# Kernel tuning notes

Measured on AMD Instinct MI355X. Metric: run time of the kernel, lower is better.

The kernel has to match this reference:

```python
import jax, jax.numpy as jnp
import numpy as np

EMBED_DIM = 1024
NUM_HEADS = 16
HEAD_DIM = EMBED_DIM // NUM_HEADS
BATCH = 4
SEQ = 2048


def setup_inputs() -> dict:
    key = jax.random.key(0)
    ks = jax.random.split(key, 9)
    s = 1.0 / np.sqrt(EMBED_DIM)
    return {
        "query": jax.random.normal(ks[0], (BATCH, SEQ, EMBED_DIM), jnp.float32),
        "Wq": jax.random.normal(ks[1], (EMBED_DIM, EMBED_DIM), jnp.float32) * s,
        "bq": jnp.zeros((EMBED_DIM,), jnp.float32),
        "Wk": jax.random.normal(ks[2], (EMBED_DIM, EMBED_DIM), jnp.float32) * s,
        "bk": jnp.zeros((EMBED_DIM,), jnp.float32),
        "Wv": jax.random.normal(ks[3], (EMBED_DIM, EMBED_DIM), jnp.float32) * s,
        "bv": jnp.zeros((EMBED_DIM,), jnp.float32),
        "Wo": jax.random.normal(ks[4], (EMBED_DIM, EMBED_DIM), jnp.float32) * s,
        "bo": jnp.zeros((EMBED_DIM,), jnp.float32),
    }


def reference(query, Wq, bq, Wk, bk, Wv, bv, Wo, bo):
    bsz, seq, embed_dim = query.shape
    scaling = HEAD_DIM ** (-0.5)
    # projections (torch Linear: x @ W.T + b)
    q = (query @ Wq.T + bq) * scaling
    k = query @ Wk.T + bk
    v = query @ Wv.T + bv
    # [b, h, s, d]
    q = q.reshape(bsz, seq, NUM_HEADS, HEAD_DIM).transpose(0, 2, 1, 3)
    k = k.reshape(bsz, seq, NUM_HEADS, HEAD_DIM).transpose(0, 2, 1, 3)
    v = v.reshape(bsz, seq, NUM_HEADS, HEAD_DIM).transpose(0, 2, 1, 3)
    # full [b, h, s, s] scores (faithful to the naive original)
    scores = jnp.einsum("bhqd,bhkd->bhqk", q, k)
    causal = jnp.tril(jnp.ones((seq, seq), bool))  # [s, s]
    scores = jnp.where(causal[None, None], scores, -jnp.inf)
    probs = jax.nn.softmax(scores, axis=-1)
    attn = jnp.einsum("bhqk,bhkd->bhqd", probs, v)
    attn = attn.transpose(0, 2, 1, 3).reshape(bsz, seq, embed_dim)
    return attn @ Wo.T + bo
```

## Files before the change

kernel.cpp:

```cpp
#include <hip/hip_runtime.h>
#include <stdint.h>

typedef unsigned short u16;
typedef __attribute__((ext_vector_type(8))) __bf16 bf16x8;
typedef __attribute__((ext_vector_type(4))) float f32x4;

#define SEQL 2048
#define NHEADS 16
#define HDIM 64
#define BSZ 4
#define EMB 1024
#define MROWS (BSZ * SEQL)
#define LOG2E 1.44269504088896f
#define NKT 32

__device__ __forceinline__ u16 f2bf(float f) {
  union { float f; uint32_t u; } v; v.f = f;
  return (u16)((v.u + 0x7fffu + ((v.u >> 16) & 1u)) >> 16);
}

__device__ __forceinline__ void g2l(const u16* g, u16* l) {
  __builtin_amdgcn_global_load_lds(
      (__attribute__((address_space(1))) void*)(g),
      (__attribute__((address_space(3))) void*)(l), 16, 0, 0);
}

__device__ __forceinline__ void cvt8(const float* __restrict__ in, u16* __restrict__ out, int i) {
  float4 a = *(const float4*)(in + i);
  float4 b = *(const float4*)(in + i + 4);
  uint4 o;
  o.x = f2bf(a.x) | ((uint32_t)f2bf(a.y) << 16);
  o.y = f2bf(a.z) | ((uint32_t)f2bf(a.w) << 16);
  o.z = f2bf(b.x) | ((uint32_t)f2bf(b.y) << 16);
  o.w = f2bf(b.z) | ((uint32_t)f2bf(b.w) << 16);
  *(uint4*)(out + i) = o;
}

#define XN (MROWS * EMB)
__global__ void cvt_all(const float* __restrict__ query,
                        const float* __restrict__ w0, const float* __restrict__ w1,
                        const float* __restrict__ w2, const float* __restrict__ w3,
                        u16* __restrict__ Xb, u16* __restrict__ Wqb) {
  int i = (blockIdx.x * blockDim.x + threadIdx.x) * 8;
  if (i < XN) {
    cvt8(query, Xb, i);
  } else {
    int j = i - XN;
    int w = j >> 20;
    int jj = j & 1048575;
    const float* src = w == 0 ? w0 : w == 1 ? w1 : w == 2 ? w2 : w3;
    cvt8(src, Wqb + ((size_t)w << 20), jj);
  }
}

#define GBODY3(WSTR, RBUF, DOPF, PFT, WBUF)                                         \
  {                                                                                 \
    asm volatile("s_waitcnt " WSTR ::: "memory");                                   \
    __builtin_amdgcn_sched_barrier(0);                                              \
    __builtin_amdgcn_s_barrier();                                                   \
    __builtin_amdgcn_sched_barrier(0);                                              \
    if (DOPF) {                                                                     \
      u16* d = lds + (WBUF) * 12288;                                                \
      g2l(Agb + (PFT) * 32, d + tid * 8);                                           \
      g2l(Bgb0 + (PFT) * 32, d + 4096 + tid * 8);                                   \
      g2l(Bgb1 + (PFT) * 32, d + 8192 + tid * 8);                                   \
    }                                                                               \
    const u16* Ab = lds + (RBUF) * 12288;                                           \
    const u16* Bb = Ab + 4096;                                                      \
    bf16x8 af[4], bfr[4];                                                           \
    _Pragma("unroll") for (int i = 0; i < 4; ++i) {                                 \
      af[i] = *(const bf16x8*)(Ab + (wr * 64 + i * 16 + lrow) * 32 + kg);           \
      bfr[i] = *(const bf16x8*)(Bb + (wc * 64 + i * 16 + lrow) * 32 + kg);          \
    }                                                                               \
    __builtin_amdgcn_s_setprio(1);                                                  \
    _Pragma("unroll") for (int mi = 0; mi < 4; ++mi)                                \
      _Pragma("unroll") for (int ni = 0; ni < 4; ++ni)                              \
        acc[mi][ni] =                                                               \
            __builtin_amdgcn_mfma_f32_16x16x32_bf16(af[mi], bfr[ni], acc[mi][ni],   \
                                                    0, 0, 0);                       \
    __builtin_amdgcn_s_setprio(0);                                                  \
  }

__device__ __forceinline__ void gemm_core256(const u16* __restrict__ A,
                                             const u16* __restrict__ B,
                                             int m0, int n0, u16* lds,
                                             f32x4 acc[4][4]) {
  const int tid = threadIdx.x;
  const int lane = tid & 63, wid = tid >> 6;
  const int wr = wid >> 2, wc = wid & 3;
  const int lrow = lane & 15, kg = (lane >> 4) * 8;
  const int srow = tid >> 2, scolE = (tid & 3) * 8;

  const u16* Agb  = A + (size_t)(m0 + srow) * EMB + scolE;
  const u16* Bgb0 = B + (size_t)(n0 + srow) * EMB + scolE;
  const u16* Bgb1 = B + (size_t)(n0 + 128 + srow) * EMB + scolE;

#pragma unroll
  for (int t = 0; t < 2; ++t) {
    u16* d = lds + t * 12288;
    g2l(Agb + t * 32, d + tid * 8);
    g2l(Bgb0 + t * 32, d + 4096 + tid * 8);
    g2l(Bgb1 + t * 32, d + 8192 + tid * 8);
  }

  int rb = 0;
#pragma unroll 1
  for (int kt = 0; kt < NKT - 2; ++kt) {
    int wb = rb + 2; if (wb >= 3) wb -= 3;
    GBODY3("vmcnt(3)", rb, true, kt + 2, wb)
    ++rb; if (rb == 3) rb = 0;
  }
  GBODY3("vmcnt(3)", rb, false, 0, 0)
  { int rb2 = rb + 1; if (rb2 == 3) rb2 = 0;
    GBODY3("vmcnt(0)", rb2, false, 0, 0) }
}

__global__ __launch_bounds__(512, 4) void gemm_qkv3(
    const u16* __restrict__ X, const u16* __restrict__ Wcat,
    const float* __restrict__ bq, const float* __restrict__ bk, const float* __restrict__ bv,
    u16* __restrict__ Qb, u16* __restrict__ Kb, u16* __restrict__ Vt) {
  __shared__ u16 lds[3 * 12288];
  const int orig = blockIdx.x;
  const int virt = (orig & 7) * 96 + (orig >> 3);
  const int mt = virt / 12, nt = virt % 12;

  const f32x4 fzero = {0.f, 0.f, 0.f, 0.f};
  f32x4 acc[4][4];
#pragma unroll
  for (int i = 0; i < 4; ++i)
#pragma unroll
    for (int j = 0; j < 4; ++j) acc[i][j] = fzero;

  gemm_core256(X, Wcat, mt * 128, nt * 256, lds, acc);

  const int tid = threadIdx.x, lane = tid & 63, wid = tid >> 6;
  const int wr = wid >> 2, wc = wid & 3;
  const int lrow = lane & 15, g = lane >> 4;
  const int which = nt >> 2;
  const float* bias = which == 0 ? bq : which == 1 ? bk : bv;
  const float scale = which == 0 ? 0.125f * LOG2E : 1.0f;

  if (which == 2) {
#pragma unroll
    for (int mi = 0; mi < 4; ++mi)
#pragma unroll
      for (int ni = 0; ni < 4; ++ni) {
        int n = nt * 256 + wc * 64 + ni * 16 + lrow;
        int nn = n & 1023;
        float bs = bias[nn];
        int h = nn >> 6, d = nn & 63;
        int m0r = mt * 128 + wr * 64 + mi * 16 + g * 4;
        int b = m0r >> 11, s = m0r & 2047;
        union { u16 s4[4]; uint2 u; } o;
#pragma unroll
        for (int r = 0; r < 4; ++r) o.s4[r] = f2bf(acc[mi][ni][r] + bs);
        *(uint2*)(Vt + ((size_t)(b * NHEADS + h) * HDIM + d) * SEQL + s) = o.u;
      }
  } else {
    u16* Ob = which == 0 ? Qb : Kb;
#pragma unroll
    for (int mi = 0; mi < 4; ++mi)
#pragma unroll
      for (int ni = 0; ni < 4; ++ni) {
        int n = nt * 256 + wc * 64 + ni * 16 + lrow;
        int nn = n & 1023;
        float bs = bias[nn];
        int h = nn >> 6, d = nn & 63;
#pragma unroll
        for (int r = 0; r < 4; ++r) {
          int m = mt * 128 + wr * 64 + mi * 16 + g * 4 + r;
          int b = m >> 11, s = m & 2047;
          float v = (acc[mi][ni][r] + bs) * scale;
          Ob[(size_t)((b * NHEADS + h) * SEQL + s) * HDIM + d] = f2bf(v);
        }
      }
  }
}

__global__ __launch_bounds__(512, 4) void gemm_out2(
    const u16* __restrict__ Ain, const u16* __restrict__ Wo,
    const float* __restrict__ bo, float* __restrict__ out) {
  __shared__ u16 lds[3 * 12288];
  const int orig = blockIdx.x;
  const int virt = (orig & 7) * 32 + (orig >> 3);
  const int mt = virt >> 2, nt = virt & 3;

  const f32x4 fzero = {0.f, 0.f, 0.f, 0.f};
  f32x4 acc[4][4];
#pragma unroll
  for (int i = 0; i < 4; ++i)
#pragma unroll
    for (int j = 0; j < 4; ++j) acc[i][j] = fzero;

  gemm_core256(Ain, Wo, mt * 128, nt * 256, lds, acc);

  const int tid = threadIdx.x, lane = tid & 63, wid = tid >> 6;
  const int wr = wid >> 2, wc = wid & 3;
  const int lrow = lane & 15, g = lane >> 4;
#pragma unroll
  for (int mi = 0; mi < 4; ++mi)
#pragma unroll
    for (int ni = 0; ni < 4; ++ni) {
      int n = nt * 256 + wc * 64 + ni * 16 + lrow;
      float bs = bo[n];
#pragma unroll
      for (int r = 0; r < 4; ++r) {
        int m = mt * 128 + wr * 64 + mi * 16 + g * 4 + r;
        out[(size_t)m * EMB + n] = acc[mi][ni][r] + bs;
      }
    }
}

__device__ __forceinline__ int swz(int row, int colE) {
  return row * 64 + (colE ^ ((row & 7) << 3));
}

__global__ __launch_bounds__(512, 4) void attn6_kernel(
    const u16* __restrict__ Qb, const u16* __restrict__ Kb, const u16* __restrict__ Vt,
    u16* __restrict__ Ab) {
  __shared__ u16 Ks[2][64 * 64];
  __shared__ u16 Vs[2][64 * 64];

  const int bid = blockIdx.x;
  const int qa  = bid >> 6;
  const int bh  = bid & 63;

  const int tid = threadIdx.x, lane = tid & 63, wid = tid >> 6;
  const int lrow = lane & 15, g = lane >> 4, kg = g * 8;

  const u16* Qbh = Qb + (size_t)bh * SEQL * HDIM;
  const u16* Kbh = Kb + (size_t)bh * SEQL * HDIM;
  const u16* Vbh = Vt + (size_t)bh * HDIM * SEQL;

  const int srow = tid >> 3;
  const int sce  = (tid & 7) * 8;

  const f32x4 fzero = {0.f, 0.f, 0.f, 0.f};
  const int b = bh >> 4, h = bh & 15;

#pragma unroll 1
  for (int ph = 0; ph < 2; ++ph) {
    const int qt = ph ? (15 - qa) : qa;
    const int q0 = qt * 128;
    const int NT = 2 * (qt + 1);

    const int qrow = q0 + wid * 16 + lrow;
    const bf16x8 qf0 = *(const bf16x8*)(Qbh + (size_t)qrow * HDIM + kg);
    const bf16x8 qf1 = *(const bf16x8*)(Qbh + (size_t)qrow * HDIM + 32 + kg);

    float m_run = -1e30f, l_run = 0.f;
    f32x4 accO[4];
#pragma unroll
    for (int d = 0; d < 4; ++d) accO[d] = fzero;

    {
      uint4 k0 = *(const uint4*)(Kbh + (size_t)srow * HDIM + sce);
      uint4 v0 = *(const uint4*)(Vbh + (size_t)srow * SEQL + sce);
      *(uint4*)(&Ks[0][swz(srow, sce)]) = k0;
      *(uint4*)(&Vs[0][swz(srow, sce)]) = v0;
    }
    __syncthreads();

    for (int t = 0; t < NT; ++t) {
      const int cur = t & 1;
      const int kv0 = t * 64;
      const bool pf = (t + 1 < NT);
      uint4 k0, v0;
      if (pf) {
        const int kvn = kv0 + 64;
        k0 = *(const uint4*)(Kbh + (size_t)(kvn + srow) * HDIM + sce);
        v0 = *(const uint4*)(Vbh + (size_t)srow * SEQL + kvn + sce);
      }

      f32x4 sacc[4];
      __builtin_amdgcn_s_setprio(1);
#pragma unroll
      for (int kb = 0; kb < 4; ++kb) {
        bf16x8 kfa = *(const bf16x8*)(&Ks[cur][swz(kb * 16 + lrow, kg)]);
        bf16x8 kfb = *(const bf16x8*)(&Ks[cur][swz(kb * 16 + lrow, 32 + kg)]);
        f32x4 z = fzero;
        z = __builtin_amdgcn_mfma_f32_16x16x32_bf16(kfa, qf0, z, 0, 0, 0);
        z = __builtin_amdgcn_mfma_f32_16x16x32_bf16(kfb, qf1, z, 0, 0, 0);
        sacc[kb] = z;
      }
      __builtin_amdgcn_s_setprio(0);

      if (kv0 + 63 > q0 + wid * 16) {
#pragma unroll
        for (int kb = 0; kb < 4; ++kb)
#pragma unroll
          for (int r = 0; r < 4; ++r)
            if (kv0 + kb * 16 + g * 4 + r > qrow) sacc[kb][r] = -1e30f;
      }

      float mx = sacc[0][0];
#pragma unroll
      for (int kb = 0; kb < 4; ++kb)
#pragma unroll
        for (int r = 0; r < 4; ++r) mx = fmaxf(mx, sacc[kb][r]);
      mx = fmaxf(mx, __shfl_xor(mx, 16));
      mx = fmaxf(mx, __shfl_xor(mx, 32));

      if (!__all(mx <= m_run + 8.f)) {
        const float mnew = fmaxf(m_run, mx);
        const float sc = __builtin_amdgcn_exp2f(m_run - mnew);
        m_run = mnew;
        l_run *= sc;
#pragma unroll
        for (int d = 0; d < 4; ++d) accO[d] *= sc;
      }

      bf16x8 pa[2];
      float ls = 0.f;
#pragma unroll
      for (int kb = 0; kb < 4; ++kb)
#pragma unroll
        for (int r = 0; r < 4; ++r) {
          float p = __builtin_amdgcn_exp2f(sacc[kb][r] - m_run);
          ls += p;
          pa[kb >> 1][(kb & 1) * 4 + r] = (__bf16)p;
        }
      l_run += ls;

      __builtin_amdgcn_s_setprio(1);
#pragma unroll
      for (int ks = 0; ks < 2; ++ks)
#pragma unroll
        for (int d = 0; d < 4; ++d) {
          union { ushort4 h2[2]; bf16x8 v; } vf;
          vf.h2[0] = *(const ushort4*)(&Vs[cur][swz(d * 16 + lrow, ks * 32 + g * 4)]);
          vf.h2[1] = *(const ushort4*)(&Vs[cur][swz(d * 16 + lrow, ks * 32 + 16 + g * 4)]);
          accO[d] = __builtin_amdgcn_mfma_f32_16x16x32_bf16(vf.v, pa[ks], accO[d], 0, 0, 0);
        }
      __builtin_amdgcn_s_setprio(0);

      if (pf) {
        const int nb = cur ^ 1;
        *(uint4*)(&Ks[nb][swz(srow, sce)]) = k0;
        *(uint4*)(&Vs[nb][swz(srow, sce)]) = v0;
      }
      __syncthreads();
    }

    float l = l_run;
    l += __shfl_xor(l, 16);
    l += __shfl_xor(l, 32);
    const float inv = 1.f / l;
#pragma unroll
    for (int d = 0; d < 4; ++d) {
      union { u16 s4[4]; uint2 u; } o;
#pragma unroll
      for (int r = 0; r < 4; ++r) o.s4[r] = f2bf(accO[d][r] * inv);
      *(uint2*)(Ab + (size_t)(b * SEQL + qrow) * EMB + h * HDIM + d * 16 + g * 4) = o.u;
    }
    __syncthreads();
  }
}

extern "C" void kernel_launch(void* const* d_in, const int* in_sizes, int n_in,
                              void* d_out, int out_size, void* d_ws, size_t ws_size,
                              hipStream_t stream) {
  (void)in_sizes; (void)n_in; (void)out_size; (void)ws_size;
  const float* query = (const float*)d_in[0];
  const float* Wq = (const float*)d_in[1];
  const float* bq = (const float*)d_in[2];
  const float* Wk = (const float*)d_in[3];
  const float* bk = (const float*)d_in[4];
  const float* Wv = (const float*)d_in[5];
  const float* bv = (const float*)d_in[6];
  const float* Wo = (const float*)d_in[7];
  const float* bo = (const float*)d_in[8];
  float* out = (float*)d_out;

  const size_t MB = 1u << 20;
  char* ws = (char*)d_ws;
  u16* Xb  = (u16*)(ws);
  u16* Wqb = (u16*)(ws + 16 * MB);
  u16* Wob = (u16*)(ws + 22 * MB);
  u16* Qbf = (u16*)(ws + 24 * MB);
  u16* Kbf = (u16*)(ws + 40 * MB);
  u16* Vtg = (u16*)(ws + 56 * MB);
  u16* Ab  = Xb;

  cvt_all<<<6144, 256, 0, stream>>>(query, Wq, Wk, Wv, Wo, Xb, Wqb);
  gemm_qkv3<<<768, 512, 0, stream>>>(Xb, Wqb, bq, bk, bv, Qbf, Kbf, Vtg);
  attn6_kernel<<<512, 512, 0, stream>>>(Qbf, Kbf, Vtg, Ab);
  gemm_out2<<<256, 512, 0, stream>>>(Ab, Wob, bo, out);
}
```

Baseline: 158.9 us.

## Switch QKV GEMM to double-buffered LDS pipeline for higher occupancy

The QKV projection GEMM moves from a triple-buffered LDS pipeline (prefetch distance 2) to a double-buffered one (prefetch distance 1), cutting shared memory per block from 72KB to 48KB. Launch bounds rise from 4 to 6 waves per SIMD so more blocks can be resident per CU. The tradeoff is that each iteration now waits with vmcnt(0) on the next tile load, which exposes more global-load latency per block in the hope that the extra resident blocks hide it.

```diff
diff --git a/kernel.cpp b/kernel.cpp
--- a/kernel.cpp
+++ b/kernel.cpp
@@ -53,19 +53,9 @@
   }
 }
 
-#define GBODY3(WSTR, RBUF, DOPF, PFT, WBUF)                                         \
+#define GFRAGS_MFMA(RBASE)                                                          \
   {                                                                                 \
-    asm volatile("s_waitcnt " WSTR ::: "memory");                                   \
-    __builtin_amdgcn_sched_barrier(0);                                              \
-    __builtin_amdgcn_s_barrier();                                                   \
-    __builtin_amdgcn_sched_barrier(0);                                              \
-    if (DOPF) {                                                                     \
-      u16* d = lds + (WBUF) * 12288;                                                \
-      g2l(Agb + (PFT) * 32, d + tid * 8);                                           \
-      g2l(Bgb0 + (PFT) * 32, d + 4096 + tid * 8);                                   \
-      g2l(Bgb1 + (PFT) * 32, d + 8192 + tid * 8);                                   \
-    }                                                                               \
-    const u16* Ab = lds + (RBUF) * 12288;                                           \
+    const u16* Ab = (RBASE);                                                        \
     const u16* Bb = Ab + 4096;                                                      \
     bf16x8 af[4], bfr[4];                                                           \
     _Pragma("unroll") for (int i = 0; i < 4; ++i) {                                 \
@@ -81,6 +71,21 @@
     __builtin_amdgcn_s_setprio(0);                                                  \
   }
 
+#define GBODY3(WSTR, RBUF, DOPF, PFT, WBUF)                                         \
+  {                                                                                 \
+    asm volatile("s_waitcnt " WSTR ::: "memory");                                   \
+    __builtin_amdgcn_sched_barrier(0);                                              \
+    __builtin_amdgcn_s_barrier();                                                   \
+    __builtin_amdgcn_sched_barrier(0);                                              \
+    if (DOPF) {                                                                     \
+      u16* d = lds + (WBUF) * 12288;                                                \
+      g2l(Agb + (PFT) * 32, d + tid * 8);                                           \
+      g2l(Bgb0 + (PFT) * 32, d + 4096 + tid * 8);                                   \
+      g2l(Bgb1 + (PFT) * 32, d + 8192 + tid * 8);                                   \
+    }                                                                               \
+    GFRAGS_MFMA(lds + (RBUF) * 12288)                                               \
+  }
+
 __device__ __forceinline__ void gemm_core256(const u16* __restrict__ A,
                                              const u16* __restrict__ B,
                                              int m0, int n0, u16* lds,
@@ -115,11 +120,45 @@
     GBODY3("vmcnt(0)", rb2, false, 0, 0) }
 }
 
-__global__ __launch_bounds__(512, 4) void gemm_qkv3(
+__device__ __forceinline__ void gemm_core256_d2(const u16* __restrict__ A,
+                                                const u16* __restrict__ B,
+                                                int m0, int n0, u16* lds,
+                                                f32x4 acc[4][4]) {
+  const int tid = threadIdx.x;
+  const int lane = tid & 63, wid = tid >> 6;
+  const int wr = wid >> 2, wc = wid & 3;
+  const int lrow = lane & 15, kg = (lane >> 4) * 8;
+  const int srow = tid >> 2, scolE = (tid & 3) * 8;
+
+  const u16* Agb  = A + (size_t)(m0 + srow) * EMB + scolE;
+  const u16* Bgb0 = B + (size_t)(n0 + srow) * EMB + scolE;
+  const u16* Bgb1 = B + (size_t)(n0 + 128 + srow) * EMB + scolE;
+
+  g2l(Agb, lds + tid * 8);
+  g2l(Bgb0, lds + 4096 + tid * 8);
+  g2l(Bgb1, lds + 8192 + tid * 8);
+
+#pragma unroll 1
+  for (int kt = 0; kt < NKT; ++kt) {
+    asm volatile("s_waitcnt vmcnt(0)" ::: "memory");
+    __builtin_amdgcn_sched_barrier(0);
+    __builtin_amdgcn_s_barrier();
+    __builtin_amdgcn_sched_barrier(0);
+    if (kt + 1 < NKT) {
+      u16* d = lds + ((kt + 1) & 1) * 12288;
+      g2l(Agb + (kt + 1) * 32, d + tid * 8);
+      g2l(Bgb0 + (kt + 1) * 32, d + 4096 + tid * 8);
+      g2l(Bgb1 + (kt + 1) * 32, d + 8192 + tid * 8);
+    }
+    GFRAGS_MFMA(lds + (kt & 1) * 12288)
+  }
+}
+
+__global__ __launch_bounds__(512, 6) void gemm_qkv3(
     const u16* __restrict__ X, const u16* __restrict__ Wcat,
     const float* __restrict__ bq, const float* __restrict__ bk, const float* __restrict__ bv,
     u16* __restrict__ Qb, u16* __restrict__ Kb, u16* __restrict__ Vt) {
-  __shared__ u16 lds[3 * 12288];
+  __shared__ u16 lds[2 * 12288];
   const int orig = blockIdx.x;
   const int virt = (orig & 7) * 96 + (orig >> 3);
   const int mt = virt / 12, nt = virt % 12;
@@ -131,7 +170,7 @@
 #pragma unroll
     for (int j = 0; j < 4; ++j) acc[i][j] = fzero;
 
-  gemm_core256(X, Wcat, mt * 128, nt * 256, lds, acc);
+  gemm_core256_d2(X, Wcat, mt * 128, nt * 256, lds, acc);
 
   const int tid = threadIdx.x, lane = tid & 63, wid = tid >> 6;
   const int wr = wid >> 2, wc = wid & 3;
```

New measurement: 531.3 us. 234% more time.
